# Kernel optimization log

Hardware: AMD Instinct MI355X
Metric: run time of the kernel (lower is better)

The kernel has to match this reference:

```python
import jax, jax.numpy as jnp
import numpy as np
from jax import lax

# dims
N, CIN, COUT, CI, T, V = 128, 64, 64, 16, 128, 25
SS, ST = 3, 2  # num_subset_S, num_subset_T
BN_EPS = 1e-5
LRELU = 0.1


def _bn(x, p):
    # x: [N,C,T,V]; p: [4,C] = (gamma, beta, running_mean, running_var), eval-mode BN
    g, b, m, v = p
    inv = g / jnp.sqrt(v + BN_EPS)
    return (x - m[:, None, None]) * inv[:, None, None] + b[:, None, None]


def _c1x1(x, w, b):
    # 1x1 Conv2d: x [N,C,T,V], w [O,C], b [O]
    return jnp.einsum('nctv,oc->notv', x, w) + b[None, :, None, None]


def _lrelu(x):
    return jnp.where(x >= 0, x, LRELU * x)


def _bn_params(c):
    return jnp.stack([jnp.ones(c, jnp.float32), jnp.zeros(c, jnp.float32),
                      jnp.zeros(c, jnp.float32), jnp.ones(c, jnp.float32)])


def setup_inputs() -> dict:
    key = jax.random.key(0)
    ks = jax.random.split(key, 12)
    d = {}
    d['x'] = jax.random.normal(ks[0], (N, CIN, T, V), jnp.float32)
    # spatial attention projections
    d['w_in_s'] = jax.random.normal(ks[1], (2 * SS * CI, CIN), jnp.float32) * 0.1
    d['b_in_s'] = jnp.zeros((2 * SS * CI,), jnp.float32)
    d['alphas'] = jnp.ones((1, SS, 1, 1), jnp.float32)
    d['att0s'] = jnp.ones((1, SS, V, V), jnp.float32) / V
    d['w_out_s'] = jax.random.normal(ks[2], (COUT, SS * CIN), jnp.float32) * 0.05
    d['b_out_s'] = jnp.zeros((COUT,), jnp.float32)
    d['bn_out_s'] = _bn_params(COUT)
    d['w_ff_s'] = jax.random.normal(ks[3], (COUT, COUT), jnp.float32) * 0.1
    d['b_ff_s'] = jnp.zeros((COUT,), jnp.float32)
    d['bn_ff_s'] = _bn_params(COUT)
    # temporal attention projections (directed)
    d['w_in_t'] = jax.random.normal(ks[4], (4 * ST * CI, COUT), jnp.float32) * 0.1
    d['b_in_t'] = jnp.zeros((4 * ST * CI,), jnp.float32)
    d['alphat_f'] = jnp.ones((1, ST, 1, 1), jnp.float32)
    d['alphat_b'] = jnp.ones((1, ST, 1, 1), jnp.float32)
    d['w_out_t'] = jax.random.normal(ks[5], (COUT, 2 * ST * COUT), jnp.float32) * 0.05
    d['b_out_t'] = jnp.zeros((COUT,), jnp.float32)
    d['bn_out_t'] = _bn_params(COUT)
    d['w_ff_t'] = jax.random.normal(ks[6], (COUT, COUT), jnp.float32) * 0.1
    d['b_ff_t'] = jnp.zeros((COUT,), jnp.float32)
    d['bn_ff_t'] = _bn_params(COUT)
    # TCN extension (7x1 temporal conv)
    d['w_tcn'] = jax.random.normal(ks[7], (COUT, COUT, 7, 1), jnp.float32) * 0.03
    d['b_tcn'] = jnp.zeros((COUT,), jnp.float32)
    d['bn_tcn'] = _bn_params(COUT)
    return d


def _forward(x, w_in_s, b_in_s, alphas, att0s, w_out_s, b_out_s, bn_out_s,
             w_ff_s, b_ff_s, bn_ff_s, w_in_t, b_in_t, alphat_f, alphat_b,
             w_out_t, b_out_t, bn_out_t, w_ff_t, b_ff_t, bn_ff_t,
             w_tcn, b_tcn, bn_tcn):
    n, c, t, v = x.shape
    # ---- spatial attention ----
    qk = _c1x1(x, w_in_s, b_in_s).reshape(n, 2 * SS, CI, t, v)
    q, k = qk[:, :SS], qk[:, SS:]
    # atts buffer is zeros; attention = tanh(QK/(ci*T))*alpha + attention0s
    attn = jnp.tanh(jnp.einsum('nsctu,nsctv->nsuv', q, k) / (CI * t)) * alphas + att0s
    y = jnp.einsum('nctu,nsuv->nsctv', x, attn).reshape(n, SS * c, t, v)
    y = _bn(_c1x1(y, w_out_s, b_out_s), bn_out_s)
    y = _lrelu(x + y)            # downs1 = identity
    y2 = _bn(_c1x1(y, w_ff_s, b_ff_s), bn_ff_s)
    y = _lrelu(x + y2)           # downs2 = identity
    # ---- temporal attention (directed) ----
    qk = _c1x1(y, w_in_t, b_in_t).reshape(n, 4 * ST, CI, t, v)
    q_f, q_b = qk[:, :ST], qk[:, ST:2 * ST]
    k_f, k_b = qk[:, 2 * ST:3 * ST], qk[:, 3 * ST:]
    bmask = jnp.triu(jnp.ones((t, t), x.dtype))
    fmask = bmask.T
    a_b = jnp.tanh(jnp.einsum('nsctv,nscqv->nstq', q_b, k_b) / (CI * v)) * alphat_b * bmask
    a_f = jnp.tanh(jnp.einsum('nsctv,nscqv->nstq', q_f, k_f) / (CI * v)) * alphat_f * fmask
    z_f = jnp.einsum('nctv,nstq->nscqv', y, a_f).reshape(n, ST * COUT, t, v)
    z_b = jnp.einsum('nctv,nstq->nscqv', y, a_b).reshape(n, ST * COUT, t, v)
    z = jnp.concatenate([z_f, z_b], axis=1)
    z = _bn(_c1x1(z, w_out_t, b_out_t), bn_out_t)
    z = _lrelu(y + z)            # downt1 = identity
    z2 = _bn(_c1x1(z, w_ff_t, b_ff_t), bn_ff_t)
    z = _lrelu(y + z2)           # downt2 = identity
    # ---- TCN extension: residual 7x1 temporal conv, downt3 = identity ----
    tcn = lax.conv_general_dilated(z, w_tcn, (1, 1), ((3, 3), (0, 0)),
                                   dimension_numbers=('NCHW', 'OIHW', 'NCHW'))
    tcn = _bn(tcn + b_tcn[None, :, None, None], bn_tcn)
    z = _lrelu(z + tcn)
    return z


def reference(x, w_in_s, b_in_s, alphas, att0s, w_out_s, b_out_s, bn_out_s,
              w_ff_s, b_ff_s, bn_ff_s, w_in_t, b_in_t, alphat_f, alphat_b,
              w_out_t, b_out_t, bn_out_t, w_ff_t, b_ff_t, bn_ff_t,
              w_tcn, b_tcn, bn_tcn):
    return _forward(x, w_in_s, b_in_s, alphas, att0s, w_out_s, b_out_s, bn_out_s,
                    w_ff_s, b_ff_s, bn_ff_s, w_in_t, b_in_t, alphat_f, alphat_b,
                    w_out_t, b_out_t, bn_out_t, w_ff_t, b_ff_t, bn_ff_t,
                    w_tcn, b_tcn, bn_tcn)
```

## Files before the change

### kernel.cpp

```cpp
#include <hip/hip_runtime.h>
#include <math.h>

#define NN   128
#define TTc  128
#define VVc  25
#define TV   3200
#define BN_EPS 1e-5f

typedef __attribute__((ext_vector_type(8))) short bf8;
typedef __attribute__((ext_vector_type(4))) short s4;
typedef __attribute__((ext_vector_type(4))) float f4;

#define MFMA(a,b,c) __builtin_amdgcn_mfma_f32_16x16x32_bf16(a,b,c,0,0,0)

__device__ __forceinline__ float lrelu(float a){ return a>=0.f ? a : 0.1f*a; }
__device__ __forceinline__ short f2bs(float f){
    union{float f; unsigned u;} x; x.f = f;
    unsigned r = x.u + 0x7FFF + ((x.u>>16)&1);
    return (short)(r>>16);
}
__device__ __forceinline__ float b2f(short s){
    union{unsigned u; float f;} x; x.u = ((unsigned)(unsigned short)s)<<16; return x.f;
}
__device__ __forceinline__ s4 packf4(float a,float b,float c,float d){
    s4 r; r.x=f2bs(a); r.y=f2bs(b); r.z=f2bs(c); r.w=f2bs(d); return r;
}


__global__ __launch_bounds__(256) void k_prep(
    const float* __restrict__ w_in_s, const float* __restrict__ w_out_s,
    const float* __restrict__ w_ff_s, const float* __restrict__ w_in_t,
    const float* __restrict__ w_out_t, const float* __restrict__ w_ff_t,
    const float* __restrict__ w_tcn, short* __restrict__ wb)
{
    const int total = 51200 + 64*448;
    for (int i = blockIdx.x*256 + threadIdx.x; i < total; i += gridDim.x*256) {
        float v;
        if      (i < 6144)  v = w_in_s[i];
        else if (i < 18432) v = w_out_s[i-6144];
        else if (i < 22528) v = w_ff_s[i-18432];
        else if (i < 30720) v = w_in_t[i-22528];
        else if (i < 47104) v = w_out_t[i-30720];
        else if (i < 51200) v = w_ff_t[i-47104];
        else { int j=i-51200; int o=j/448; int r=j%448; int dt=r>>6; int c=r&63;
               v = w_tcn[(o*64+c)*7 + dt]; }
        wb[i] = f2bs(v);
    }
}

__global__ __launch_bounds__(256) void k_x2b(const float* __restrict__ x, short* __restrict__ XB)
{
    const int n = blockIdx.x >> 4, tc = blockIdx.x & 15, t0 = tc*8;
    const int tid = threadIdx.x;
    __shared__ float xs[64][203];
    const float* xb = x + (size_t)n*204800 + t0*25;
    for (int i = tid; i < 64*200; i += 256) { int c=i/200, p=i%200; xs[c][p] = xb[(size_t)c*3200 + p]; }
    __syncthreads();
    short* ob = XB + (size_t)n*204800 + t0*25*64;
    for (int i = tid; i < 200*16; i += 256) {
        const int p = i>>4, c0 = (i&15)<<2;
        *(s4*)&ob[p*64 + c0] = packf4(xs[c0][p], xs[c0+1][p], xs[c0+2][p], xs[c0+3][p]);
    }
}

__global__ __launch_bounds__(256) void k_attn_s(
    const short* __restrict__ XB, const short* __restrict__ wb,
    const float* __restrict__ b_in_s, const float* __restrict__ alphas,
    const float* __restrict__ att0s, short* __restrict__ attnB)
{
    const int n = blockIdx.x / 3, s = blockIdx.x % 3;
    const int tid = threadIdx.x, w = tid>>6, lane = tid&63, lr = lane&15, lq = lane>>4;
    __shared__ short ys[208][72];
    __shared__ short qkl[208][40];
    __shared__ short wsl[32][72];
    __shared__ float bl[32];

    for (int i = tid; i < 32*8; i += 256) {
        const int cl = i>>3, seg = i&7;
        const int row = (cl < 16) ? (s*16 + cl) : (48 + s*16 + (cl-16));
        *(bf8*)&wsl[cl][seg*8] = *(const bf8*)&wb[row*64 + seg*8];
    }
    if (tid < 32) {
        const int row = (tid < 16) ? (s*16 + tid) : (48 + s*16 + (tid-16));
        bl[tid] = b_in_s[row];
    }

    const int mt = w>>1, sn = w&1;
    f4 acc = {0.f,0.f,0.f,0.f};

    for (int ch = 0; ch < 16; ++ch) {
        __syncthreads();
        for (int i = tid; i < 208*8; i += 256) {
            const int row = i>>3, seg = i&7;
            bf8 val = {0,0,0,0,0,0,0,0};
            if (row < 200)
                val = *(const bf8*)&XB[((size_t)n*3200 + ch*200 + row)*64 + seg*8];
            *(bf8*)&ys[row][seg*8] = val;
        }
        __syncthreads();
        for (int nn = 0; nn < 4; ++nn) {
            const int nt2 = w + nn*4;
            if (nt2 >= 13) break;
            const bf8 b0 = *(const bf8*)&ys[nt2*16+lr][lq*8];
            const bf8 b1 = *(const bf8*)&ys[nt2*16+lr][32+lq*8];
            for (int mt2 = 0; mt2 < 2; ++mt2) {
                f4 pa = {0.f,0.f,0.f,0.f};
                const bf8 a0 = *(const bf8*)&wsl[mt2*16+lr][lq*8];
                const bf8 a1 = *(const bf8*)&wsl[mt2*16+lr][32+lq*8];
                pa = MFMA(a0,b0,pa); pa = MFMA(a1,b1,pa);
                const int px = nt2*16+lr, c0 = mt2*16+lq*4;
                *(s4*)&qkl[px][c0] =
                    packf4(pa.x+bl[c0], pa.y+bl[c0+1], pa.z+bl[c0+2], pa.w+bl[c0+3]);
            }
        }
        __syncthreads();
        for (int ks = 0; ks < 4; ++ks) {
            const int tl = ks*2 + (lq>>1);
            const bf8 af = *(const bf8*)&qkl[tl*25 + mt*16+lr][(lq&1)*8];
            const bf8 bf = *(const bf8*)&qkl[tl*25 + sn*16+lr][16 + (lq&1)*8];
            acc = MFMA(af, bf, acc);
        }
    }
    const float alpha = alphas[s];
    const int v = sn*16 + lr, u0 = mt*16 + lq*4;
    float r[4];
    #pragma unroll
    for (int j = 0; j < 4; ++j) {
        const int u = u0 + j;
        const float a = (j==0)?acc.x:((j==1)?acc.y:((j==2)?acc.z:acc.w));
        r[j] = (u < 25 && v < 25)
             ? tanhf(a*(1.f/2048.f))*alpha + att0s[s*625 + u*25 + v] : 0.f;
    }
    *(s4*)&attnB[(size_t)n*3072 + v*96 + s*32 + u0] = packf4(r[0],r[1],r[2],r[3]);
}

__global__ __launch_bounds__(256) void k_spatial(
    const short* __restrict__ XB, const short* __restrict__ attnB, const short* __restrict__ wb,
    const float* __restrict__ b_out, const float* __restrict__ bn_out,
    const float* __restrict__ b_ff,  const float* __restrict__ bn_ff,
    short* __restrict__ Y)
{
    const int n = blockIdx.x >> 5, tc = blockIdx.x & 31, t0 = tc*4;
    const int tid = threadIdx.x;
    const int w = tid>>6, lane = tid&63, lr = lane&15, lq = lane>>4;
    __shared__ short xs[4][32][72];
    __shared__ short wlo[64][200];
    __shared__ short wlf[64][72];
    __shared__ short ab[32][104];
    __shared__ short gsT[4][64][104];
    __shared__ short y1[4][32][72];
    __shared__ float sc1s[64], sh1s[64], sc2s[64], sh2s[64];

    for (int i = tid; i < 4*32*8; i += 256) {
        const int row = i>>3, seg = i&7, tl = row>>5, uv = row&31;
        bf8 val = {0,0,0,0,0,0,0,0};
        if (uv < 25) val = *(const bf8*)&XB[((size_t)n*3200 + (t0+tl)*25 + uv)*64 + seg*8];
        *(bf8*)&xs[tl][uv][seg*8] = val;
    }
    for (int i = tid; i < 64*24; i += 256) {
        const int o = i/24, seg = i%24;
        *(bf8*)&wlo[o][seg*8] = *(const bf8*)&wb[6144 + o*192 + seg*8];
    }
    for (int i = tid; i < 64*8; i += 256) {
        const int o = i>>3, seg = i&7;
        *(bf8*)&wlf[o][seg*8] = *(const bf8*)&wb[18432 + o*64 + seg*8];
    }
    for (int i = tid; i < 32*12; i += 256) {
        const int v = i/12, seg = i%12;
        *(bf8*)&ab[v][seg*8] = *(const bf8*)&attnB[(size_t)n*3072 + v*96 + seg*8];
    }
    if (tid < 64) {
        float g=bn_out[tid], bb=bn_out[64+tid], m=bn_out[128+tid], vv=bn_out[192+tid];
        float inv = g*rsqrtf(vv+BN_EPS);
        sc1s[tid]=inv; sh1s[tid]=(b_out[tid]-m)*inv+bb;
        g=bn_ff[tid]; bb=bn_ff[64+tid]; m=bn_ff[128+tid]; vv=bn_ff[192+tid];
        inv = g*rsqrtf(vv+BN_EPS);
        sc2s[tid]=inv; sh2s[tid]=(b_ff[tid]-m)*inv+bb;
    }
    __syncthreads();

    const int t = t0 + w;
    for (int s = 0; s < 3; ++s) {
        for (int mt = 0; mt < 2; ++mt) {
            const bf8 a0 = *(const bf8*)&xs[w][mt*16+lr][lq*8];
            const bf8 a1 = *(const bf8*)&xs[w][mt*16+lr][32+lq*8];
            for (int nt = 0; nt < 4; ++nt) {
                f4 acc = {0.f,0.f,0.f,0.f};
                const bf8 b0 = *(const bf8*)&wlo[nt*16+lr][s*64 + lq*8];
                const bf8 b1 = *(const bf8*)&wlo[nt*16+lr][s*64 + 32 + lq*8];
                acc = MFMA(a0,b0,acc); acc = MFMA(a1,b1,acc);
                const int o = nt*16+lr, u0 = mt*16+lq*4;
                *(s4*)&gsT[w][o][s*32+u0] = packf4(acc.x,acc.y,acc.z,acc.w);
            }
        }
    }
    for (int mt = 0; mt < 4; ++mt) {
        const bf8 a0 = *(const bf8*)&gsT[w][mt*16+lr][lq*8];
        const bf8 a1 = *(const bf8*)&gsT[w][mt*16+lr][32+lq*8];
        const bf8 a2 = *(const bf8*)&gsT[w][mt*16+lr][64+lq*8];
        for (int nt = 0; nt < 2; ++nt) {
            f4 acc = {0.f,0.f,0.f,0.f};
            const bf8 b0 = *(const bf8*)&ab[nt*16+lr][lq*8];
            const bf8 b1 = *(const bf8*)&ab[nt*16+lr][32+lq*8];
            const bf8 b2 = *(const bf8*)&ab[nt*16+lr][64+lq*8];
            acc = MFMA(a0,b0,acc); acc = MFMA(a1,b1,acc); acc = MFMA(a2,b2,acc);
            const int v = nt*16+lr, o0 = mt*16+lq*4;
            const s4 xr = *(const s4*)&xs[w][v][o0];
            const float r0 = lrelu(acc.x*sc1s[o0  ]+sh1s[o0  ]+b2f(xr.x));
            const float r1 = lrelu(acc.y*sc1s[o0+1]+sh1s[o0+1]+b2f(xr.y));
            const float r2 = lrelu(acc.z*sc1s[o0+2]+sh1s[o0+2]+b2f(xr.z));
            const float r3 = lrelu(acc.w*sc1s[o0+3]+sh1s[o0+3]+b2f(xr.w));
            *(s4*)&y1[w][v][o0] = packf4(r0,r1,r2,r3);
        }
    }
    for (int mt = 0; mt < 4; ++mt) {
        const bf8 a0 = *(const bf8*)&wlf[mt*16+lr][lq*8];
        const bf8 a1 = *(const bf8*)&wlf[mt*16+lr][32+lq*8];
        for (int nt = 0; nt < 2; ++nt) {
            f4 acc = {0.f,0.f,0.f,0.f};
            const bf8 b0 = *(const bf8*)&y1[w][nt*16+lr][lq*8];
            const bf8 b1 = *(const bf8*)&y1[w][nt*16+lr][32+lq*8];
            acc = MFMA(a0,b0,acc); acc = MFMA(a1,b1,acc);
            const int v = nt*16+lr, o0 = mt*16+lq*4;
            if (v < 25) {
                const s4 xr = *(const s4*)&xs[w][v][o0];
                const float r0 = lrelu(acc.x*sc2s[o0  ]+sh2s[o0  ]+b2f(xr.x));
                const float r1 = lrelu(acc.y*sc2s[o0+1]+sh2s[o0+1]+b2f(xr.y));
                const float r2 = lrelu(acc.z*sc2s[o0+2]+sh2s[o0+2]+b2f(xr.z));
                const float r3 = lrelu(acc.w*sc2s[o0+3]+sh2s[o0+3]+b2f(xr.w));
                *(s4*)&Y[((size_t)n*3200 + t*25 + v)*64 + o0] = packf4(r0,r1,r2,r3);
            }
        }
    }
}

__global__ __launch_bounds__(256) void k_qkt(
    const short* __restrict__ Y, const short* __restrict__ wb,
    const float* __restrict__ b_in_t, short* __restrict__ qkt)
{
    const int n = blockIdx.x >> 5, tc = blockIdx.x & 31, t0 = tc*4;
    const int tid = threadIdx.x;
    const int w = tid>>6, lane = tid&63, lr = lane&15, lq = lane>>4;
    __shared__ short ys[4][32][72];
    __shared__ short wi[128][72];
    for (int i = tid; i < 4*32*8; i += 256) {
        const int row = i>>3, seg = i&7, tl = row>>5, v = row&31;
        bf8 val = {0,0,0,0,0,0,0,0};
        if (v < 25) val = *(const bf8*)&Y[((size_t)n*3200 + (t0+tl)*25 + v)*64 + seg*8];
        *(bf8*)&ys[tl][v][seg*8] = val;
    }
    for (int i = tid; i < 128*8; i += 256) {
        const int o = i>>3, seg = i&7;
        *(bf8*)&wi[o][seg*8] = *(const bf8*)&wb[22528 + o*64 + seg*8];
    }
    __syncthreads();
    for (int mi = 0; mi < 2; ++mi) {
        const int mt = w*2+mi, tl = mt>>1, vh = mt&1;
        const bf8 a0 = *(const bf8*)&ys[tl][vh*16+lr][lq*8];
        const bf8 a1 = *(const bf8*)&ys[tl][vh*16+lr][32+lq*8];
        for (int nt = 0; nt < 8; ++nt) {
            f4 acc = {0.f,0.f,0.f,0.f};
            const bf8 b0 = *(const bf8*)&wi[nt*16+lr][lq*8];
            const bf8 b1 = *(const bf8*)&wi[nt*16+lr][32+lq*8];
            acc = MFMA(a0,b0,acc); acc = MFMA(a1,b1,acc);
            const int oc = nt*16+lr, v0 = vh*16+lq*4, t = t0+tl;
            const float bias = b_in_t[oc];
            const size_t base = (size_t)n*409600 + (size_t)t*3200 + oc*25 + v0;
            if (v0 < 24)
                *(s4*)&qkt[base] = packf4(acc.x+bias, acc.y+bias, acc.z+bias, acc.w+bias);
            else if (v0 == 24)
                qkt[base] = f2bs(acc.x+bias);
        }
    }
}

__global__ __launch_bounds__(256) void k_score_t(
    const short* __restrict__ qkt, const float* __restrict__ alphat_f,
    const float* __restrict__ alphat_b, short* __restrict__ aT)
{
    const int n = blockIdx.x >> 2, ds = blockIdx.x & 3, dir = ds>>1, s = ds&1;
    const int qoff = dir*32 + s*16, koff = 64 + dir*32 + s*16;
    const float alpha = dir ? alphat_b[s] : alphat_f[s];
    const int tid = threadIdx.x, w = tid>>6, lane = tid&63, lr = lane&15, lq = lane>>4;
    const short* qb = qkt + (size_t)n*409600;
    short* ao = aT + (size_t)(n*4+ds)*16384;
    const bf8 zf = {0,0,0,0,0,0,0,0};
    for (int ni = 0; ni < 2; ++ni) {
        const int nt = w*2+ni;
        for (int mt = 0; mt < 8; ++mt) {
            const int q = nt*16+lr, t0r = mt*16+lq*4;
            const bool skip = (dir==0) ? (mt < nt) : (mt > nt);
            if (skip) { s4 z = {0,0,0,0}; *(s4*)&ao[q*128 + t0r] = z; continue; }
            f4 acc = {0.f,0.f,0.f,0.f};
            for (int ks = 0; ks < 13; ++ks) {
                bf8 af, bf;
                if (ks==12 && lq>=2) { af = zf; bf = zf; }
                else {
                    af = *(const bf8*)&qb[(size_t)(mt*16+lr)*3200 + qoff*25 + ks*32 + lq*8];
                    bf = *(const bf8*)&qb[(size_t)(nt*16+lr)*3200 + koff*25 + ks*32 + lq*8];
                }
                acc = MFMA(af, bf, acc);
            }
            float r[4];
            #pragma unroll
            for (int j = 0; j < 4; ++j) {
                const int tt = t0r + j;
                const bool ok = (dir==0) ? (tt >= q) : (tt <= q);
                const float a = (j==0)?acc.x:((j==1)?acc.y:((j==2)?acc.z:acc.w));
                r[j] = ok ? tanhf(a*(1.f/400.f))*alpha : 0.f;
            }
            *(s4*)&ao[q*128 + t0r] = packf4(r[0],r[1],r[2],r[3]);
        }
    }
}

__global__ __launch_bounds__(256) void k_tagg(
    const short* __restrict__ Y, const short* __restrict__ wb,
    const short* __restrict__ aT, short* __restrict__ U)
{
    const int n = blockIdx.x / 25, v = blockIdx.x % 25;
    const int tid = threadIdx.x, w = tid>>6, lane = tid&63, lr = lane&15, lq = lane>>4;
    __shared__ short ys[128][72];
    __shared__ short wolds[64][72];
    __shared__ short pt[64][136];
    __shared__ short ats[128][136];

    for (int i = tid; i < 128*8; i += 256) {
        const int t = i>>3, seg = i&7;
        *(bf8*)&ys[t][seg*8] = *(const bf8*)&Y[((size_t)n*3200 + t*25 + v)*64 + seg*8];
    }

    f4 acc[8];
    #pragma unroll
    for (int nt = 0; nt < 8; ++nt) { acc[nt].x=0.f; acc[nt].y=0.f; acc[nt].z=0.f; acc[nt].w=0.f; }

    for (int ds = 0; ds < 4; ++ds) {
        const int dir = ds>>1;
        __syncthreads();
        for (int i = tid; i < 64*8; i += 256) {
            const int o = i>>3, seg = i&7;
            *(bf8*)&wolds[o][seg*8] = *(const bf8*)&wb[30720 + o*256 + ds*64 + seg*8];
        }
        for (int i = tid; i < 128*16; i += 256) {
            const int q = i>>4, seg = i&15;
            *(bf8*)&ats[q][seg*8] = *(const bf8*)&aT[(size_t)(n*4+ds)*16384 + q*128 + seg*8];
        }
        __syncthreads();
        {
            const bf8 b0 = *(const bf8*)&wolds[w*16+lr][lq*8];
            const bf8 b1 = *(const bf8*)&wolds[w*16+lr][32+lq*8];
            #pragma unroll
            for (int tt = 0; tt < 8; ++tt) {
                f4 p = {0.f,0.f,0.f,0.f};
                const bf8 a0 = *(const bf8*)&ys[tt*16+lr][lq*8];
                const bf8 a1 = *(const bf8*)&ys[tt*16+lr][32+lq*8];
                p = MFMA(a0,b0,p); p = MFMA(a1,b1,p);
                *(s4*)&pt[w*16+lr][tt*16+lq*4] = packf4(p.x,p.y,p.z,p.w);
            }
        }
        __syncthreads();
        bf8 af[4];
        #pragma unroll
        for (int ks = 0; ks < 4; ++ks)
            af[ks] = *(const bf8*)&pt[w*16+lr][ks*32+lq*8];
        #pragma unroll
        for (int nt = 0; nt < 8; ++nt) {
            #pragma unroll
            for (int ks = 0; ks < 4; ++ks) {
                const bool skip = (dir==0) ? (ks*32+31 < nt*16) : (ks*32 > nt*16+15);
                if (skip) continue;
                const bf8 bf = *(const bf8*)&ats[nt*16+lr][ks*32+lq*8];
                acc[nt] = MFMA(af[ks], bf, acc[nt]);
            }
        }
    }
    #pragma unroll
    for (int nt = 0; nt < 8; ++nt) {
        const int q = nt*16+lr, o0 = w*16+lq*4;
        *(s4*)&U[((size_t)(n*128+q)*25 + v)*64 + o0] =
            packf4(acc[nt].x, acc[nt].y, acc[nt].z, acc[nt].w);
    }
}

__global__ __launch_bounds__(256) void k_temporal(
    const short* __restrict__ U, short* __restrict__ Y, const short* __restrict__ wb,
    const float* __restrict__ b_out, const float* __restrict__ bn_out,
    const float* __restrict__ b_ff,  const float* __restrict__ bn_ff)
{
    const int n = blockIdx.x >> 5, qc = blockIdx.x & 31, q0 = qc*4;
    const int tid = threadIdx.x, w = tid>>6, lane = tid&63, lr = lane&15, lq = lane>>4;
    __shared__ short zs[112][72];
    __shared__ short z1[112][72];
    __shared__ short zout[112][72];
    __shared__ short wf[64][72];
    __shared__ float sc1s[64], sh1s[64], sc2s[64], sh2s[64];
    if (tid < 64) {
        float g=bn_out[tid], bb=bn_out[64+tid], m=bn_out[128+tid], vv=bn_out[192+tid];
        float inv = g*rsqrtf(vv+BN_EPS);
        sc1s[tid]=inv; sh1s[tid]=(b_out[tid]-m)*inv+bb;
        g=bn_ff[tid]; bb=bn_ff[64+tid]; m=bn_ff[128+tid]; vv=bn_ff[192+tid];
        inv = g*rsqrtf(vv+BN_EPS);
        sc2s[tid]=inv; sh2s[tid]=(b_ff[tid]-m)*inv+bb;
    }
    for (int i = tid; i < 64*8; i += 256) {
        const int o = i>>3, seg = i&7;
        *(bf8*)&wf[o][seg*8] = *(const bf8*)&wb[47104 + o*64 + seg*8];
    }
    __syncthreads();
    for (int i = tid; i < 112*8; i += 256) {
        const int row = i>>3, seg = i&7;
        bf8 yv = {0,0,0,0,0,0,0,0}, zv = yv;
        if (row < 100) {
            const int q = q0 + row/25, v = row%25;
            yv = *(const bf8*)&Y[((size_t)n*3200 + q*25 + v)*64 + seg*8];
            const bf8 uv = *(const bf8*)&U[((size_t)(n*128+q)*25 + v)*64 + seg*8];
            #pragma unroll
            for (int j = 0; j < 8; ++j) {
                const int o = seg*8+j;
                zv[j] = f2bs(lrelu(b2f(yv[j]) + b2f(uv[j])*sc1s[o] + sh1s[o]));
            }
        }
        *(bf8*)&zs[row][seg*8] = yv;
        *(bf8*)&z1[row][seg*8] = zv;
    }
    __syncthreads();
    const bf8 a0 = *(const bf8*)&wf[w*16+lr][lq*8];
    const bf8 a1 = *(const bf8*)&wf[w*16+lr][32+lq*8];
    for (int nt = 0; nt < 7; ++nt) {
        f4 acc = {0.f,0.f,0.f,0.f};
        const bf8 b0 = *(const bf8*)&z1[nt*16+lr][lq*8];
        const bf8 b1 = *(const bf8*)&z1[nt*16+lr][32+lq*8];
        acc = MFMA(a0,b0,acc); acc = MFMA(a1,b1,acc);
        const int px = nt*16+lr, o0 = w*16+lq*4;
        const s4 yr = *(const s4*)&zs[px][o0];
        const float r0 = lrelu(acc.x*sc2s[o0  ]+sh2s[o0  ]+b2f(yr.x));
        const float r1 = lrelu(acc.y*sc2s[o0+1]+sh2s[o0+1]+b2f(yr.y));
        const float r2 = lrelu(acc.z*sc2s[o0+2]+sh2s[o0+2]+b2f(yr.z));
        const float r3 = lrelu(acc.w*sc2s[o0+3]+sh2s[o0+3]+b2f(yr.w));
        *(s4*)&zout[px][o0] = packf4(r0,r1,r2,r3);
    }
    __syncthreads();
    for (int i = tid; i < 100*8; i += 256) {
        const int row = i>>3, seg = i&7;
        *(bf8*)&Y[((size_t)n*3200 + q0*25 + row)*64 + seg*8] = *(const bf8*)&zout[row][seg*8];
    }
}

__global__ __launch_bounds__(256, 2) void k_tcn(
    const short* __restrict__ Y, const short* __restrict__ wb,
    const float* __restrict__ b, const float* __restrict__ bn,
    float* __restrict__ out)
{
    const int n = blockIdx.x >> 5, tc = (blockIdx.x >> 1) & 15, oh = blockIdx.x & 1;
    const int t0 = tc*8;
    const int tid = threadIdx.x, w = tid>>6, lane = tid&63, lr = lane&15, lq = lane>>4;
    __shared__ short zs[352][72];
    __shared__ float scs[32], shs[32];

    bf8 af[2][14];
    #pragma unroll
    for (int mt = 0; mt < 2; ++mt)
        #pragma unroll
        for (int st = 0; st < 14; ++st)
            af[mt][st] = *(const bf8*)&wb[51200 + (oh*32 + mt*16 + lr)*448 + st*32 + lq*8];

    if (tid < 32) {
        const int o = oh*32 + tid;
        const float g=bn[o], bb=bn[64+o], m=bn[128+o], vv=bn[192+o];
        const float inv = g*rsqrtf(vv+BN_EPS);
        scs[tid]=inv; shs[tid]=(b[o]-m)*inv+bb;
    }
    for (int i = tid; i < 352*8; i += 256) {
        const int row = i>>3, seg = i&7;
        bf8 val = {0,0,0,0,0,0,0,0};
        if (row < 350) {
            const int tlp = row/25, v = row%25, t = t0 - 3 + tlp;
            if (t >= 0 && t < 128)
                val = *(const bf8*)&Y[((size_t)n*3200 + t*25 + v)*64 + seg*8];
        }
        *(bf8*)&zs[row][seg*8] = val;
    }
    __syncthreads();
    for (int nn = 0; nn < 4; ++nn) {
        const int nt = w + nn*4;
        if (nt >= 13) break;
        bf8 bfr[14];
        #pragma unroll
        for (int st = 0; st < 14; ++st)
            bfr[st] = *(const bf8*)&zs[nt*16 + lr + (st>>1)*25][(st&1)*32 + lq*8];
        f4 ac[2][4];
        #pragma unroll
        for (int m2 = 0; m2 < 2; ++m2)
            #pragma unroll
            for (int j = 0; j < 4; ++j) { ac[m2][j].x=0.f; ac[m2][j].y=0.f; ac[m2][j].z=0.f; ac[m2][j].w=0.f; }
        #pragma unroll
        for (int st = 0; st < 14; ++st) {
            ac[0][st&3] = MFMA(af[0][st], bfr[st], ac[0][st&3]);
            ac[1][st&3] = MFMA(af[1][st], bfr[st], ac[1][st&3]);
        }
        const int px = nt*16+lr;
        if (px < 200) {
            #pragma unroll
            for (int mt = 0; mt < 2; ++mt) {
                const float ax = ac[mt][0].x+ac[mt][1].x+ac[mt][2].x+ac[mt][3].x;
                const float ay = ac[mt][0].y+ac[mt][1].y+ac[mt][2].y+ac[mt][3].y;
                const float az = ac[mt][0].z+ac[mt][1].z+ac[mt][2].z+ac[mt][3].z;
                const float aw = ac[mt][0].w+ac[mt][1].w+ac[mt][2].w+ac[mt][3].w;
                const int o0l = mt*16+lq*4;
                const s4 zr = *(const s4*)&zs[px+75][oh*32+o0l];
                float* ob = out + (size_t)n*204800 + (size_t)(oh*32+o0l)*3200 + t0*25 + px;
                ob[0]    = lrelu(ax*scs[o0l  ]+shs[o0l  ]+b2f(zr.x));
                ob[3200] = lrelu(ay*scs[o0l+1]+shs[o0l+1]+b2f(zr.y));
                ob[6400] = lrelu(az*scs[o0l+2]+shs[o0l+2]+b2f(zr.z));
                ob[9600] = lrelu(aw*scs[o0l+3]+shs[o0l+3]+b2f(zr.w));
            }
        }
    }
}

extern "C" void kernel_launch(void* const* d_in, const int* in_sizes, int n_in,
                              void* d_out, int out_size, void* d_ws, size_t ws_size,
                              hipStream_t stream) {
    const float* x        = (const float*)d_in[0];
    const float* w_in_s   = (const float*)d_in[1];
    const float* b_in_s   = (const float*)d_in[2];
    const float* alphas   = (const float*)d_in[3];
    const float* att0s    = (const float*)d_in[4];
    const float* w_out_s  = (const float*)d_in[5];
    const float* b_out_s  = (const float*)d_in[6];
    const float* bn_out_s = (const float*)d_in[7];
    const float* w_ff_s   = (const float*)d_in[8];
    const float* b_ff_s   = (const float*)d_in[9];
    const float* bn_ff_s  = (const float*)d_in[10];
    const float* w_in_t   = (const float*)d_in[11];
    const float* b_in_t   = (const float*)d_in[12];
    const float* alphat_f = (const float*)d_in[13];
    const float* alphat_b = (const float*)d_in[14];
    const float* w_out_t  = (const float*)d_in[15];
    const float* b_out_t  = (const float*)d_in[16];
    const float* bn_out_t = (const float*)d_in[17];
    const float* w_ff_t   = (const float*)d_in[18];
    const float* b_ff_t   = (const float*)d_in[19];
    const float* bn_ff_t  = (const float*)d_in[20];
    const float* w_tcn    = (const float*)d_in[21];
    const float* b_tcn    = (const float*)d_in[22];
    const float* bn_tcn   = (const float*)d_in[23];
    float* out = (float*)d_out;
    char* ws = (char*)d_ws;

    short* wb    = (short*)(ws + 0);
    short* attnB = (short*)(ws + 4102144);
    short* Y     = (short*)(ws + 4888576);
    short* aT    = (short*)(ws + 57317376);
    short* XB    = (short*)(ws + 74094592);
    short* QKT   = (short*)(ws + 74094592);
    short* U     = (short*)(ws + 74094592 + 52428800);

    k_prep<<<64, 256, 0, stream>>>(w_in_s, w_out_s, w_ff_s, w_in_t, w_out_t, w_ff_t, w_tcn, wb);
    k_x2b<<<2048, 256, 0, stream>>>(x, XB);
    k_attn_s<<<NN * 3, 256, 0, stream>>>(XB, wb, b_in_s, alphas, att0s, attnB);
    k_spatial<<<4096, 256, 0, stream>>>(XB, attnB, wb, b_out_s, bn_out_s, b_ff_s, bn_ff_s, Y);
    k_qkt<<<4096, 256, 0, stream>>>(Y, wb, b_in_t, QKT);
    k_score_t<<<512, 256, 0, stream>>>(QKT, alphat_f, alphat_b, aT);
    k_tagg<<<NN * 25, 256, 0, stream>>>(Y, wb, aT, U);
    k_temporal<<<4096, 256, 0, stream>>>(U, Y, wb, b_out_t, bn_out_t, b_ff_t, bn_ff_t);
    k_tcn<<<4096, 256, 0, stream>>>(Y, wb, b_tcn, bn_tcn, out);
}
```

Before: 770.0 us.

## Restructure temporal aggregation to read attention from registers and double-buffer projections

The temporal aggregation kernel no longer stages the attention matrix and output weights in shared memory. Each wave loads its attention rows and weight fragments straight from global memory into registers. The MFMA roles are swapped so each wave owns two query tiles across all output channels, and the projected tile is double-buffered to remove one barrier per subset. LDS use drops and launch bounds now request 3 blocks per SM. The trade-off is more register pressure and scalar strided 2-byte stores to U, which may coalesce poorly.

```diff
diff --git a/kernel.cpp b/kernel.cpp
--- a/kernel.cpp
+++ b/kernel.cpp
@@ -314,71 +314,93 @@
     }
 }
 
-__global__ __launch_bounds__(256) void k_tagg(
+__global__ __launch_bounds__(256, 3) void k_tagg(
     const short* __restrict__ Y, const short* __restrict__ wb,
     const short* __restrict__ aT, short* __restrict__ U)
 {
     const int n = blockIdx.x / 25, v = blockIdx.x % 25;
     const int tid = threadIdx.x, w = tid>>6, lane = tid&63, lr = lane&15, lq = lane>>4;
     __shared__ short ys[128][72];
-    __shared__ short wolds[64][72];
-    __shared__ short pt[64][136];
-    __shared__ short ats[128][136];
+    __shared__ short pt[2][64][136];
 
     for (int i = tid; i < 128*8; i += 256) {
         const int t = i>>3, seg = i&7;
         *(bf8*)&ys[t][seg*8] = *(const bf8*)&Y[((size_t)n*3200 + t*25 + v)*64 + seg*8];
     }
-
-    f4 acc[8];
+    bf8 wr[4][2];
     #pragma unroll
-    for (int nt = 0; nt < 8; ++nt) { acc[nt].x=0.f; acc[nt].y=0.f; acc[nt].z=0.f; acc[nt].w=0.f; }
-
     for (int ds = 0; ds < 4; ++ds) {
-        const int dir = ds>>1;
-        __syncthreads();
-        for (int i = tid; i < 64*8; i += 256) {
-            const int o = i>>3, seg = i&7;
-            *(bf8*)&wolds[o][seg*8] = *(const bf8*)&wb[30720 + o*256 + ds*64 + seg*8];
-        }
-        for (int i = tid; i < 128*16; i += 256) {
-            const int q = i>>4, seg = i&15;
-            *(bf8*)&ats[q][seg*8] = *(const bf8*)&aT[(size_t)(n*4+ds)*16384 + q*128 + seg*8];
-        }
-        __syncthreads();
+        wr[ds][0] = *(const bf8*)&wb[30720 + (w*16+lr)*256 + ds*64 + lq*8];
+        wr[ds][1] = *(const bf8*)&wb[30720 + (w*16+lr)*256 + ds*64 + 32 + lq*8];
+    }
+
+    f4 acc[2][4];
+    #pragma unroll
+    for (int mi = 0; mi < 2; ++mi)
+        #pragma unroll
+        for (int nt = 0; nt < 4; ++nt) { acc[mi][nt].x=0.f; acc[mi][nt].y=0.f; acc[mi][nt].z=0.f; acc[mi][nt].w=0.f; }
+
+    __syncthreads();
+
+    #pragma unroll
+    for (int ds = 0; ds < 4; ++ds) {
+        const int dir = ds>>1, buf = ds&1;
+        bf8 ar[2][4];
+        #pragma unroll
+        for (int mi = 0; mi < 2; ++mi) {
+            const int qt = 2*w + mi;
+            #pragma unroll
+            for (int ks = 0; ks < 4; ++ks) {
+                const bool skip = (dir==0) ? (ks*32+31 < qt*16) : (ks*32 > qt*16+15);
+                if (!skip)
+                    ar[mi][ks] = *(const bf8*)&aT[(size_t)(n*4+ds)*16384
+                                                  + (qt*16+lr)*128 + ks*32 + lq*8];
+            }
+        }
         {
-            const bf8 b0 = *(const bf8*)&wolds[w*16+lr][lq*8];
-            const bf8 b1 = *(const bf8*)&wolds[w*16+lr][32+lq*8];
+            const bf8 b0 = wr[ds][0], b1 = wr[ds][1];
             #pragma unroll
             for (int tt = 0; tt < 8; ++tt) {
                 f4 p = {0.f,0.f,0.f,0.f};
                 const bf8 a0 = *(const bf8*)&ys[tt*16+lr][lq*8];
                 const bf8 a1 = *(const bf8*)&ys[tt*16+lr][32+lq*8];
                 p = MFMA(a0,b0,p); p = MFMA(a1,b1,p);
-                *(s4*)&pt[w*16+lr][tt*16+lq*4] = packf4(p.x,p.y,p.z,p.w);
+                *(s4*)&pt[buf][w*16+lr][tt*16+lq*4] = packf4(p.x,p.y,p.z,p.w);
             }
         }
         __syncthreads();
-        bf8 af[4];
-        #pragma unroll
-        for (int ks = 0; ks < 4; ++ks)
-            af[ks] = *(const bf8*)&pt[w*16+lr][ks*32+lq*8];
-        #pragma unroll
-        for (int nt = 0; nt < 8; ++nt) {
-            #pragma unroll
-            for (int ks = 0; ks < 4; ++ks) {
-                const bool skip = (dir==0) ? (ks*32+31 < nt*16) : (ks*32 > nt*16+15);
-                if (skip) continue;
-                const bf8 bf = *(const bf8*)&ats[nt*16+lr][ks*32+lq*8];
-                acc[nt] = MFMA(af[ks], bf, acc[nt]);
+        #pragma unroll
+        for (int ks = 0; ks < 4; ++ks) {
+            const bool skip0 = (dir==0) ? (ks*32+31 < (2*w)*16)   : (ks*32 > (2*w)*16+15);
+            const bool skip1 = (dir==0) ? (ks*32+31 < (2*w+1)*16) : (ks*32 > (2*w+1)*16+15);
+            if (skip0 && skip1) continue;
+            bf8 bfr[4];
+            #pragma unroll
+            for (int nt = 0; nt < 4; ++nt)
+                bfr[nt] = *(const bf8*)&pt[buf][nt*16+lr][ks*32+lq*8];
+            if (!skip0) {
+                #pragma unroll
+                for (int nt = 0; nt < 4; ++nt)
+                    acc[0][nt] = MFMA(ar[0][ks], bfr[nt], acc[0][nt]);
+            }
+            if (!skip1) {
+                #pragma unroll
+                for (int nt = 0; nt < 4; ++nt)
+                    acc[1][nt] = MFMA(ar[1][ks], bfr[nt], acc[1][nt]);
             }
         }
     }
     #pragma unroll
-    for (int nt = 0; nt < 8; ++nt) {
-        const int q = nt*16+lr, o0 = w*16+lq*4;
-        *(s4*)&U[((size_t)(n*128+q)*25 + v)*64 + o0] =
-            packf4(acc[nt].x, acc[nt].y, acc[nt].z, acc[nt].w);
+    for (int mi = 0; mi < 2; ++mi) {
+        #pragma unroll
+        for (int j = 0; j < 4; ++j) {
+            const int q = (2*w+mi)*16 + lq*4 + j;
+            short* ub = &U[((size_t)(n*128+q)*25 + v)*64 + lr];
+            ub[0]  = f2bs(acc[mi][0][j]);
+            ub[16] = f2bs(acc[mi][1][j]);
+            ub[32] = f2bs(acc[mi][2][j]);
+            ub[48] = f2bs(acc[mi][3][j]);
+        }
     }
 }
 
```

Result: faster. 714.7 us (-7.2%).
